# Kernel tuning notes

Hardware: AMD Instinct MI355X
Metric: run time of the kernel (lower is better)

## Reference

```python
import jax, jax.numpy as jnp
import numpy as np

DIM = 2048
ATT_DIM = 2048
N_HEADS = 16
HEAD_DIM = ATT_DIM // N_HEADS  # 128


def setup_inputs() -> dict:
    key = jax.random.key(0)
    k1, k2, k3 = jax.random.split(key, 3)
    tgt_len = 2048
    x = jax.random.normal(k1, (tgt_len, DIM), dtype=jnp.float32)
    # nn.Linear weights: [out_features, in_features], no bias
    w_in = jax.random.normal(k2, (3 * ATT_DIM, DIM), dtype=jnp.float32) * (1.0 / np.sqrt(DIM))
    w_out = jax.random.normal(k3, (DIM, ATT_DIM), dtype=jnp.float32) * (1.0 / np.sqrt(ATT_DIM))
    return {"x": x, "w_in": w_in, "w_out": w_out, "tgt_len": tgt_len}


def reference(x, w_in, w_out, tgt_len):
    # qkv projection: Linear -> x @ W^T, then split into thirds
    qkv = x @ w_in.T                      # [T, 3*att_dim]
    q, k, v = jnp.split(qkv, 3, axis=-1)  # each [T, att_dim]
    # [T, H, Dh] -> [H, T, Dh]
    q = q.reshape(tgt_len, N_HEADS, HEAD_DIM).transpose(1, 0, 2)
    k = k.reshape(tgt_len, N_HEADS, HEAD_DIM).transpose(1, 0, 2)
    v = v.reshape(tgt_len, N_HEADS, HEAD_DIM).transpose(1, 0, 2)
    scaling = 1.0 / jnp.sqrt(jnp.asarray(HEAD_DIM, dtype=x.dtype))
    scores = jnp.einsum("htd,hsd->hts", q, k) * scaling  # [H, T, T]
    attn = jax.nn.softmax(scores, axis=-1)
    ctx = jnp.einsum("hts,hsd->htd", attn, v)             # [H, T, Dh]
    ctx = ctx.transpose(1, 0, 2).reshape(tgt_len, ATT_DIM)
    return ctx @ w_out.T                                   # [T, dim]
```

## Files before the change

### kernel.cpp

```cpp
#include <hip/hip_runtime.h>

#define T_LEN 2048
#define DIM 2048
#define NH 16
#define HD 128
#define QKV_LD 6144

typedef __attribute__((ext_vector_type(8))) short short8;
typedef __attribute__((ext_vector_type(4))) float f32x4;
typedef __attribute__((ext_vector_type(4))) float float4v;
typedef __attribute__((ext_vector_type(4))) unsigned short ushort4v;
typedef __attribute__((ext_vector_type(2))) unsigned int uint2v;

static __device__ __forceinline__ unsigned short f2bf(float f) {
  unsigned u = __builtin_bit_cast(unsigned, f);
  u += 0x7fffu + ((u >> 16) & 1u);
  return (unsigned short)(u >> 16);
}

static __device__ __forceinline__ float max3f(float a, float b, float c) {
  return fmaxf(fmaxf(a, b), c);
}

static __device__ __forceinline__ f32x4 mfma16(short8 a, short8 b, f32x4 c) {
  return __builtin_amdgcn_mfma_f32_16x16x32_bf16(a, b, c, 0, 0, 0);
}

#define GLDS16(SRC, DST)                                                            \
  __builtin_amdgcn_global_load_lds((__attribute__((address_space(1))) void*)(SRC),  \
                                   (__attribute__((address_space(3))) void*)(DST),  \
                                   16, 0, 0)

__global__ void cast_f32_bf16(const float* __restrict__ in,
                              unsigned short* __restrict__ out, int n4) {
  int i = blockIdx.x * blockDim.x + threadIdx.x;
  const int stride = gridDim.x * blockDim.x;
  for (; i < n4; i += stride) {
    float4v f = ((const float4v*)in)[i];
    ushort4v o;
    o.x = f2bf(f.x); o.y = f2bf(f.y); o.z = f2bf(f.z); o.w = f2bf(f.w);
    ((ushort4v*)out)[i] = o;
  }
}

template <int OUT_BF16>
__global__ __launch_bounds__(256) void gemm_bt_128(
    const unsigned short* __restrict__ A,
    const unsigned short* __restrict__ B,
    void* __restrict__ Cv, int M, int N, int K) {
  __shared__ unsigned short As[128 * 64];
  __shared__ unsigned short Bs[128 * 64];
  const int tid = threadIdx.x;
  const int wave = tid >> 6;
  const int lane = tid & 63;
  const int l15 = lane & 15, l16 = lane >> 4;
  const int bm = blockIdx.y * 128;
  const int bn = blockIdx.x * 128;
  const int wr = wave >> 1, wc = wave & 1;

  f32x4 acc[4][4] = {};

  int srow[4], scol[4];
#pragma unroll
  for (int i = 0; i < 4; ++i) {
    int lin = i * 4096 + tid * 16;
    int row = lin >> 7;
    int cb = lin & 127;
    srow[i] = row;
    scol[i] = (cb ^ ((row & 7) << 4)) >> 1;
  }

  for (int k0 = 0; k0 < K; k0 += 64) {
#pragma unroll
    for (int i = 0; i < 4; ++i) {
      GLDS16(A + (size_t)(bm + srow[i]) * K + k0 + scol[i], As + i * 2048 + wave * 512);
      GLDS16(B + (size_t)(bn + srow[i]) * K + k0 + scol[i], Bs + i * 2048 + wave * 512);
    }
    __syncthreads();
#pragma unroll
    for (int kk = 0; kk < 2; ++kk) {
      const int cb = kk * 64 + l16 * 16;
      short8 af[4], bfr[4];
#pragma unroll
      for (int m = 0; m < 4; ++m) {
        int row = wr * 64 + m * 16 + l15;
        af[m] = *(const short8*)((const char*)As + row * 128 + (cb ^ ((row & 7) << 4)));
      }
#pragma unroll
      for (int n = 0; n < 4; ++n) {
        int row = wc * 64 + n * 16 + l15;
        bfr[n] = *(const short8*)((const char*)Bs + row * 128 + (cb ^ ((row & 7) << 4)));
      }
#pragma unroll
      for (int m = 0; m < 4; ++m)
#pragma unroll
        for (int n = 0; n < 4; ++n)
          acc[m][n] = mfma16(af[m], bfr[n], acc[m][n]);
    }
    __syncthreads();
  }

#pragma unroll
  for (int m = 0; m < 4; ++m)
#pragma unroll
    for (int n = 0; n < 4; ++n) {
      int row = bm + wr * 64 + m * 16 + l16 * 4;
      int col = bn + wc * 64 + n * 16 + l15;
#pragma unroll
      for (int j = 0; j < 4; ++j) {
        if (OUT_BF16)
          ((unsigned short*)Cv)[(size_t)(row + j) * N + col] = f2bf(acc[m][n][j]);
        else
          ((float*)Cv)[(size_t)(row + j) * N + col] = acc[m][n][j];
      }
    }
}

__global__ __launch_bounds__(256) void transpose_v(
    const unsigned short* __restrict__ qkv, unsigned short* __restrict__ vt) {
  __shared__ unsigned short t[64 * 128];
  const int tid = threadIdx.x;
  const int h = blockIdx.y;
  const int s0 = blockIdx.x * 64;
#pragma unroll
  for (int i = 0; i < 4; ++i) {
    int lin = i * 2048 + tid * 8;
    int row = lin >> 7, col = lin & 127;
    char* dst = (char*)t + row * 256 + ((col * 2) ^ (((row >> 3) & 7) << 4));
    *(short8*)dst =
        *(const short8*)(qkv + (size_t)(s0 + row) * QKV_LD + 2 * DIM + h * HD + col);
  }
  __syncthreads();
#pragma unroll
  for (int i2 = 0; i2 < 4; ++i2) {
    int d = (tid >> 3) + i2 * 32;
    int sb = (tid & 7) * 8;
    short8 v;
#pragma unroll
    for (int j = 0; j < 8; ++j) {
      int s = sb + j;
      v[j] = *(const short*)((const char*)t + s * 256 + ((d * 2) ^ (((s >> 3) & 7) << 4)));
    }
    *(short8*)(vt + ((size_t)h * HD + d) * T_LEN + s0 + sb) = v;
  }
}

__global__ __launch_bounds__(256) void attn_fwd(
    const unsigned short* __restrict__ qkv,
    const unsigned short* __restrict__ vt,
    unsigned short* __restrict__ ctx) {
  __shared__ unsigned short Ks[64 * 128];
  __shared__ unsigned short Vs[128 * 64];
  __shared__ unsigned short Ps[4 * 16 * 64];
  const int tid = threadIdx.x;
  const int wave = tid >> 6;
  const int lane = tid & 63;
  const int l15 = lane & 15, l16 = lane >> 4;

  const int wg = blockIdx.y * 32 + blockIdx.x;
  const int swz = (wg & 7) * 64 + (wg >> 3);
  const int h = swz >> 5;
  const int q0 = (swz & 31) * 64 + wave * 16;
  const float SCL = 0.08838834764831845f * 1.4426950408889634f;

  short8 qf[4];
#pragma unroll
  for (int kk = 0; kk < 4; ++kk)
    qf[kk] = *(const short8*)(qkv + (size_t)(q0 + l15) * QKV_LD + h * HD + kk * 32 + l16 * 8);

  f32x4 acc_o[8] = {};
  float m_r = -1e30f;
  float l_r = 0.f;

  const unsigned short* kp[4];
  const unsigned short* vp[4];
#pragma unroll
  for (int i = 0; i < 4; ++i) {
    int lin = i * 4096 + tid * 16;
    int r = lin >> 8;
    int cb = lin & 255;
    kp[i] = qkv + 2048 + h * HD + (size_t)r * QKV_LD + ((cb ^ ((r & 7) << 4)) >> 1);
    r = lin >> 7;
    cb = lin & 127;
    vp[i] = vt + (size_t)h * HD * T_LEN + (size_t)r * T_LEN + ((cb ^ ((r & 7) << 4)) >> 1);
  }

  const int NT = T_LEN / 64;
  for (int t = 0; t < NT; ++t) {
#pragma unroll
    for (int i = 0; i < 4; ++i) {
      GLDS16(kp[i], Ks + i * 2048 + wave * 512);
      GLDS16(vp[i], Vs + i * 2048 + wave * 512);
      kp[i] += 64 * QKV_LD;
      vp[i] += 64;
    }
    __syncthreads();

    f32x4 st[4] = {};
#pragma unroll
    for (int c = 0; c < 4; ++c) {
#pragma unroll
      for (int kk = 0; kk < 4; ++kk) {
        int row = c * 16 + l15;
        int cb = kk * 64 + l16 * 16;
        short8 kf = *(const short8*)((const char*)Ks + row * 256 + (cb ^ ((row & 7) << 4)));
        st[c] = mfma16(kf, qf[kk], st[c]);
      }
    }

    float ma = max3f(st[0][0], st[0][1], st[0][2]);
    float mb = max3f(st[0][3], st[1][0], st[1][1]);
    float mc = max3f(st[1][2], st[1][3], st[2][0]);
    float md = max3f(st[2][1], st[2][2], st[2][3]);
    float me = max3f(st[3][0], st[3][1], st[3][2]);
    float pmax = fmaxf(max3f(ma, mb, mc), max3f(md, me, st[3][3]));
    pmax *= SCL;
    pmax = fmaxf(pmax, __shfl_xor(pmax, 16));
    pmax = fmaxf(pmax, __shfl_xor(pmax, 32));

    if (!__all(pmax - m_r <= 8.0f)) {
      float nm = fmaxf(m_r, pmax);
      float corr = __builtin_amdgcn_exp2f(m_r - nm);
      m_r = nm;
      l_r *= corr;
      float cj[4];
#pragma unroll
      for (int j = 0; j < 4; ++j) cj[j] = __shfl(corr, l16 * 4 + j);
#pragma unroll
      for (int d = 0; d < 8; ++d)
#pragma unroll
        for (int j = 0; j < 4; ++j) acc_o[d][j] *= cj[j];
    }

    float p[4][4];
#pragma unroll
    for (int c = 0; c < 4; ++c)
#pragma unroll
      for (int j = 0; j < 4; ++j)
        p[c][j] = __builtin_amdgcn_exp2f(st[c][j] * SCL - m_r);
    float s01 = (p[0][0] + p[0][1]) + (p[0][2] + p[0][3]);
    float s23 = (p[1][0] + p[1][1]) + (p[1][2] + p[1][3]);
    float s45 = (p[2][0] + p[2][1]) + (p[2][2] + p[2][3]);
    float s67 = (p[3][0] + p[3][1]) + (p[3][2] + p[3][3]);
    float tsum = (s01 + s23) + (s45 + s67);
    tsum += __shfl_xor(tsum, 16);
    tsum += __shfl_xor(tsum, 32);
    l_r += tsum;

    char* pbase = (char*)Ps + wave * 2048;
#pragma unroll
    for (int c = 0; c < 4; ++c) {
      uint2v w;
      w.x = (unsigned)f2bf(p[c][0]) | ((unsigned)f2bf(p[c][1]) << 16);
      w.y = (unsigned)f2bf(p[c][2]) | ((unsigned)f2bf(p[c][3]) << 16);
      int off = l15 * 128 + c * 32 + l16 * 8;
      *(uint2v*)(pbase + (off ^ ((l15 & 7) << 4))) = w;
    }

#pragma unroll
    for (int kk = 0; kk < 2; ++kk) {
      int cb = kk * 64 + l16 * 16;
      short8 pa = *(const short8*)(pbase + l15 * 128 + (cb ^ ((l15 & 7) << 4)));
#pragma unroll
      for (int d = 0; d < 8; ++d) {
        int row = d * 16 + l15;
        short8 vb = *(const short8*)((const char*)Vs + row * 128 + (cb ^ ((row & 7) << 4)));
        acc_o[d] = mfma16(pa, vb, acc_o[d]);
      }
    }

    __syncthreads();
  }

  float lq[4];
#pragma unroll
  for (int j = 0; j < 4; ++j) lq[j] = 1.0f / __shfl(l_r, l16 * 4 + j);
#pragma unroll
  for (int d = 0; d < 8; ++d)
#pragma unroll
    for (int j = 0; j < 4; ++j) {
      int row = q0 + l16 * 4 + j;
      int col = h * HD + d * 16 + l15;
      ctx[(size_t)row * DIM + col] = f2bf(acc_o[d][j] * lq[j]);
    }
}

extern "C" void kernel_launch(void* const* d_in, const int* in_sizes, int n_in,
                              void* d_out, int out_size, void* d_ws, size_t ws_size,
                              hipStream_t stream) {
  const float* x = (const float*)d_in[0];
  const float* w_in = (const float*)d_in[1];
  const float* w_out = (const float*)d_in[2];

  char* ws = (char*)d_ws;
  unsigned short* xbf  = (unsigned short*)(ws + 0);
  unsigned short* wibf = (unsigned short*)(ws + 8388608);
  unsigned short* wobf = (unsigned short*)(ws + 33554432);
  unsigned short* qkv  = (unsigned short*)(ws + 41943040);
  unsigned short* ctx  = (unsigned short*)(ws + 67108864);
  unsigned short* vt   = (unsigned short*)(ws + 75497472);

  cast_f32_bf16<<<2048, 256, 0, stream>>>(x, xbf, (T_LEN * DIM) / 4);
  cast_f32_bf16<<<2048, 256, 0, stream>>>(w_in, wibf, (3 * DIM * DIM) / 4);
  cast_f32_bf16<<<2048, 256, 0, stream>>>(w_out, wobf, (DIM * DIM) / 4);

  gemm_bt_128<1><<<dim3(48, 16), 256, 0, stream>>>(xbf, wibf, (void*)qkv, T_LEN, 3 * DIM, DIM);
  transpose_v<<<dim3(32, 16), 256, 0, stream>>>(qkv, vt);
  attn_fwd<<<dim3(32, 16), 256, 0, stream>>>(qkv, vt, ctx);
  gemm_bt_128<0><<<dim3(16, 16), 256, 0, stream>>>(ctx, wobf, d_out, T_LEN, DIM, DIM);
}
```

Measured before the change: 194.6 us.

## Split attention over key halves with a separate combine kernel

Result: slower. 204.1 us (+4.9%).

```diff
diff --git a/kernel.cpp b/kernel.cpp
--- a/kernel.cpp
+++ b/kernel.cpp
@@ -16,6 +16,11 @@
   unsigned u = __builtin_bit_cast(unsigned, f);
   u += 0x7fffu + ((u >> 16) & 1u);
   return (unsigned short)(u >> 16);
+}
+
+static __device__ __forceinline__ float bf2f(unsigned short u) {
+  unsigned x = ((unsigned)u) << 16;
+  return __builtin_bit_cast(float, x);
 }
 
 static __device__ __forceinline__ float max3f(float a, float b, float c) {
@@ -148,7 +153,8 @@
 __global__ __launch_bounds__(256) void attn_fwd(
     const unsigned short* __restrict__ qkv,
     const unsigned short* __restrict__ vt,
-    unsigned short* __restrict__ ctx) {
+    unsigned short* __restrict__ po,
+    float* __restrict__ ml) {
   __shared__ unsigned short Ks[64 * 128];
   __shared__ unsigned short Vs[128 * 64];
   __shared__ unsigned short Ps[4 * 16 * 64];
@@ -157,10 +163,12 @@
   const int lane = tid & 63;
   const int l15 = lane & 15, l16 = lane >> 4;
 
-  const int wg = blockIdx.y * 32 + blockIdx.x;
-  const int swz = (wg & 7) * 64 + (wg >> 3);
-  const int h = swz >> 5;
+  const int wg = blockIdx.y * 64 + blockIdx.x;
+  const int swz = (wg & 7) * 128 + (wg >> 3);
+  const int h = swz >> 6;
+  const int half = (swz >> 5) & 1;
   const int q0 = (swz & 31) * 64 + wave * 16;
+  const int s_begin = half * (T_LEN / 2);
   const float SCL = 0.08838834764831845f * 1.4426950408889634f;
 
   short8 qf[4];
@@ -179,13 +187,14 @@
     int lin = i * 4096 + tid * 16;
     int r = lin >> 8;
     int cb = lin & 255;
-    kp[i] = qkv + 2048 + h * HD + (size_t)r * QKV_LD + ((cb ^ ((r & 7) << 4)) >> 1);
+    kp[i] = qkv + 2048 + h * HD + (size_t)(s_begin + r) * QKV_LD + ((cb ^ ((r & 7) << 4)) >> 1);
     r = lin >> 7;
     cb = lin & 127;
-    vp[i] = vt + (size_t)h * HD * T_LEN + (size_t)r * T_LEN + ((cb ^ ((r & 7) << 4)) >> 1);
-  }
-
-  const int NT = T_LEN / 64;
+    vp[i] = vt + (size_t)h * HD * T_LEN + (size_t)r * T_LEN + s_begin +
+            ((cb ^ ((r & 7) << 4)) >> 1);
+  }
+
+  const int NT = (T_LEN / 2) / 64;
   for (int t = 0; t < NT; ++t) {
 #pragma unroll
     for (int i = 0; i < 4; ++i) {
@@ -197,6 +206,7 @@
     __syncthreads();
 
     f32x4 st[4] = {};
+    __builtin_amdgcn_s_setprio(1);
 #pragma unroll
     for (int c = 0; c < 4; ++c) {
 #pragma unroll
@@ -207,6 +217,7 @@
         st[c] = mfma16(kf, qf[kk], st[c]);
       }
     }
+    __builtin_amdgcn_s_setprio(0);
 
     float ma = max3f(st[0][0], st[0][1], st[0][2]);
     float mb = max3f(st[0][3], st[1][0], st[1][1]);
@@ -257,6 +268,7 @@
       *(uint2v*)(pbase + (off ^ ((l15 & 7) << 4))) = w;
     }
 
+    __builtin_amdgcn_s_setprio(1);
 #pragma unroll
     for (int kk = 0; kk < 2; ++kk) {
       int cb = kk * 64 + l16 * 16;
@@ -268,21 +280,47 @@
         acc_o[d] = mfma16(pa, vb, acc_o[d]);
       }
     }
+    __builtin_amdgcn_s_setprio(0);
 
     __syncthreads();
   }
 
-  float lq[4];
-#pragma unroll
-  for (int j = 0; j < 4; ++j) lq[j] = 1.0f / __shfl(l_r, l16 * 4 + j);
+  const size_t pbaseo = ((size_t)half * NH * T_LEN + (size_t)h * T_LEN) * HD;
 #pragma unroll
   for (int d = 0; d < 8; ++d)
 #pragma unroll
     for (int j = 0; j < 4; ++j) {
-      int row = q0 + l16 * 4 + j;
-      int col = h * HD + d * 16 + l15;
-      ctx[(size_t)row * DIM + col] = f2bf(acc_o[d][j] * lq[j]);
-    }
+      int q = q0 + l16 * 4 + j;
+      po[pbaseo + (size_t)q * HD + d * 16 + l15] = f2bf(acc_o[d][j]);
+    }
+  if (l16 == 0) {
+    size_t mlbase = ((size_t)half * NH * T_LEN + (size_t)h * T_LEN + q0 + l15) * 2;
+    ml[mlbase] = m_r;
+    ml[mlbase + 1] = l_r;
+  }
+}
+
+__global__ __launch_bounds__(256) void attn_combine(
+    const unsigned short* __restrict__ po, const float* __restrict__ ml,
+    unsigned short* __restrict__ ctx) {
+  const int g = blockIdx.x * 256 + threadIdx.x;
+  const int hq = g >> 4;
+  const int oct = g & 15;
+  const float m0 = ml[hq * 2], l0 = ml[hq * 2 + 1];
+  const float m1 = ml[NH * T_LEN * 2 + hq * 2], l1 = ml[NH * T_LEN * 2 + hq * 2 + 1];
+  const float m = fmaxf(m0, m1);
+  float a0 = __builtin_amdgcn_exp2f(m0 - m);
+  float a1 = __builtin_amdgcn_exp2f(m1 - m);
+  const float rl = 1.0f / (l0 * a0 + l1 * a1);
+  a0 *= rl; a1 *= rl;
+  const short8 o0 = *(const short8*)(po + (size_t)hq * HD + oct * 8);
+  const short8 o1 = *(const short8*)(po + (size_t)NH * T_LEN * HD + (size_t)hq * HD + oct * 8);
+  short8 w;
+#pragma unroll
+  for (int j = 0; j < 8; ++j)
+    w[j] = (short)f2bf(bf2f((unsigned short)o0[j]) * a0 + bf2f((unsigned short)o1[j]) * a1);
+  const int h = hq >> 11, q = hq & (T_LEN - 1);
+  *(short8*)(ctx + (size_t)q * DIM + h * HD + oct * 8) = w;
 }
 
 extern "C" void kernel_launch(void* const* d_in, const int* in_sizes, int n_in,
@@ -299,6 +337,8 @@
   unsigned short* qkv  = (unsigned short*)(ws + 41943040);
   unsigned short* ctx  = (unsigned short*)(ws + 67108864);
   unsigned short* vt   = (unsigned short*)(ws + 75497472);
+  unsigned short* po   = (unsigned short*)(ws + 0);
+  float*          ml   = (float*)(ws + 16777216);
 
   cast_f32_bf16<<<2048, 256, 0, stream>>>(x, xbf, (T_LEN * DIM) / 4);
   cast_f32_bf16<<<2048, 256, 0, stream>>>(w_in, wibf, (3 * DIM * DIM) / 4);
@@ -306,6 +346,7 @@
 
   gemm_bt_128<1><<<dim3(48, 16), 256, 0, stream>>>(xbf, wibf, (void*)qkv, T_LEN, 3 * DIM, DIM);
   transpose_v<<<dim3(32, 16), 256, 0, stream>>>(qkv, vt);
-  attn_fwd<<<dim3(32, 16), 256, 0, stream>>>(qkv, vt, ctx);
+  attn_fwd<<<dim3(64, 16), 256, 0, stream>>>(qkv, vt, po, ml);
+  attn_combine<<<2048, 256, 0, stream>>>(po, ml, ctx);
   gemm_bt_128<0><<<dim3(16, 16), 256, 0, stream>>>(ctx, wobf, d_out, T_LEN, DIM, DIM);
 }
```
